# Optimization experiments

Measured on AMD Instinct MI355X. Metric: run time of the kernel, lower is better.

## Reference

```python
import jax, jax.numpy as jnp
import numpy as np

K_NEIGHBORS = 32  # nsample

def setup_inputs() -> dict:
    key = jax.random.key(0)
    ks = jax.random.split(key, 16)
    B, C, N = 4, 3, 4096
    def w(k, shape):
        return jax.random.normal(k, shape, dtype=jnp.float32) * 0.05
    inp = {"x": jax.random.normal(ks[0], (B, C, N), dtype=jnp.float32)}
    # three scale MLPs share shapes -> stack along leading scale axis (s=3)
    inp["sW0"] = w(ks[1], (3, 64, 3));    inp["sb0"] = w(ks[2], (3, 64))
    inp["sW1"] = w(ks[3], (3, 64, 64));   inp["sb1"] = w(ks[4], (3, 64))
    inp["sW2"] = w(ks[5], (3, 128, 64));  inp["sb2"] = w(ks[6], (3, 128))
    inp["gW0"] = w(ks[7], (256, 384));    inp["gb0"] = w(ks[8], (256,))
    inp["gW1"] = w(ks[9], (1024, 256));   inp["gb1"] = w(ks[10], (1024,))
    inp["mW0"] = w(ks[11], (256, 1024));  inp["mb0"] = w(ks[12], (256,))
    inp["mW1"] = w(ks[13], (128, 256));   inp["mb1"] = w(ks[14], (128,))
    return inp

def _knn_idx(x, k):
    # x: [B, 3, N] channels-first points; k nearest neighbors excluding self
    pts = jnp.swapaxes(x, 1, 2)                       # [B, N, 3]
    sq = jnp.sum(pts * pts, axis=-1)                  # [B, N]
    d = sq[:, :, None] + sq[:, None, :] - 2.0 * jnp.einsum('bnc,bmc->bnm', pts, pts)
    _, idx = jax.lax.top_k(-d, k + 1)                 # nearest first (self at 0)
    return idx[:, :, 1:]                              # [B, N, k]

def reference(x, sW0, sb0, sW1, sb1, sW2, sb2, gW0, gb0, gW1, gb1, mW0, mb0, mW1, mb1):
    B, C, N = x.shape
    # radius is unused by sample_and_group_knn -> all three scales share knn idx
    idx = _knn_idx(x, K_NEIGHBORS)                    # [B, N, K]
    # gather: per-batch x[:, idx[b]] -> [B, C, N, K]
    g = jax.vmap(lambda xf, i: xf[:, i])(x, idx)
    # three shared-weight 1x1-conv MLPs, batched over scale axis s
    h = jax.nn.relu(jnp.einsum('bcnk,soc->sbonk', g, sW0) + sb0[:, None, :, None, None])
    h = jax.nn.relu(jnp.einsum('sbcnk,soc->sbonk', h, sW1) + sb1[:, None, :, None, None])
    h = jax.nn.relu(jnp.einsum('sbcnk,soc->sbonk', h, sW2) + sb2[:, None, :, None, None])
    p = jnp.max(h, axis=-1)                           # [3, B, 128, N] max over neighbors
    point = jnp.moveaxis(p, 0, 1).reshape(B, 3 * p.shape[2], N)  # concat scales -> [B, 384, N]
    gf = jax.nn.relu(jnp.einsum('bcn,oc->bon', point, gW0) + gb0[None, :, None])
    gf = jax.nn.relu(jnp.einsum('bcn,oc->bon', gf, gW1) + gb1[None, :, None])     # [B,1024,N]
    msf = jax.nn.relu(jnp.einsum('bcn,oc->bon', gf, mW0) + mb0[None, :, None])
    msf = jax.nn.relu(jnp.einsum('bcn,oc->bon', msf, mW1) + mb1[None, :, None])   # [B,128,N]
    global_feature = jnp.max(gf, axis=-1)             # [B, 1024]
    return (global_feature, msf)
```

## Files before the change

### kernel.cpp

```cpp
#include <hip/hip_runtime.h>
#include <hip/hip_bf16.h>

#define NPTS 4096
#define KNN  32

typedef __attribute__((ext_vector_type(8))) short short8;
typedef __attribute__((ext_vector_type(4))) float floatx4;
typedef unsigned short u16x2 __attribute__((ext_vector_type(2)));

__device__ __forceinline__ unsigned short f2bf(float f) {
    unsigned u = __float_as_uint(f);
    u = (u + 0x7FFFu + ((u >> 16) & 1u)) >> 16;
    return (unsigned short)u;
}

__global__ __launch_bounds__(256) void prep_all(
    const float* __restrict__ x, float4* __restrict__ pts4,
    const float* __restrict__ gW0, const float* __restrict__ gW1,
    const float* __restrict__ mW0, const float* __restrict__ mW1,
    const float* __restrict__ sW1, const float* __restrict__ sW2,
    unsigned short* __restrict__ Wb0, unsigned short* __restrict__ Wb1,
    unsigned short* __restrict__ Wb2, unsigned short* __restrict__ Wb3,
    unsigned short* __restrict__ Wb4, unsigned short* __restrict__ Wb5)
{
    const int blk = blockIdx.x, t = threadIdx.x;
    if (blk < 64) {
        const int i = blk * 256 + t;
        const int b = i >> 12, n = i & (NPTS - 1);
        const float* xb = x + (size_t)b * 3 * NPTS;
        const float qx = xb[n], qy = xb[NPTS + n], qz = xb[2 * NPTS + n];
        pts4[i] = make_float4(qx, qy, qz, qx * qx + qy * qy + qz * qz);
    } else {
        const int wi = (blk - 64) * 256 + t;
        float v; unsigned short* dst;
        if (wi < 98304)       { v = gW0[wi];          dst = Wb0 + wi; }
        else if (wi < 360448) { v = gW1[wi - 98304];  dst = Wb1 + (wi - 98304); }
        else if (wi < 622592) { v = mW0[wi - 360448]; dst = Wb2 + (wi - 360448); }
        else if (wi < 655360) { v = mW1[wi - 622592]; dst = Wb3 + (wi - 622592); }
        else if (wi < 667648) { v = sW1[wi - 655360]; dst = Wb4 + (wi - 655360); }
        else                  { v = sW2[wi - 667648]; dst = Wb5 + (wi - 667648); }
        *dst = f2bf(v);
    }
}

__global__ __launch_bounds__(256) void knn_kernel13(const float4* __restrict__ pts4,
                                                    int* __restrict__ knn_out)
{
    __shared__ unsigned sred[2][4];
    __shared__ unsigned long long C[256];
    __shared__ unsigned ccnt;

    const int t = threadIdx.x, wid = t >> 6, lane = t & 63;
    const int q = blockIdx.x, b = q >> 12, n = q & (NPTS - 1);
    const float4* P = pts4 + ((size_t)b << 12);
    const float4 s = P[n];
    const float px = s.x, py = s.y, pz = s.z, sqn = s.w;

    if (t == 0) ccnt = 0u;

    unsigned key[16];
    #pragma unroll
    for (int g = 0; g < 4; ++g) {
        float4 c0 = P[((g * 4 + 0) << 8) + t];
        float4 c1 = P[((g * 4 + 1) << 8) + t];
        float4 c2 = P[((g * 4 + 2) << 8) + t];
        float4 c3 = P[((g * 4 + 3) << 8) + t];
        float d0 = (sqn + c0.w) - 2.0f * (px * c0.x + py * c0.y + pz * c0.z);
        float d1 = (sqn + c1.w) - 2.0f * (px * c1.x + py * c1.y + pz * c1.z);
        float d2 = (sqn + c2.w) - 2.0f * (px * c2.x + py * c2.y + pz * c2.z);
        float d3 = (sqn + c3.w) - 2.0f * (px * c3.x + py * c3.y + pz * c3.z);
        unsigned u0 = __float_as_uint(d0), u1 = __float_as_uint(d1);
        unsigned u2 = __float_as_uint(d2), u3 = __float_as_uint(d3);
        key[g * 4 + 0] = (u0 & 0x80000000u) ? ~u0 : (u0 | 0x80000000u);
        key[g * 4 + 1] = (u1 & 0x80000000u) ? ~u1 : (u1 | 0x80000000u);
        key[g * 4 + 2] = (u2 & 0x80000000u) ? ~u2 : (u2 | 0x80000000u);
        key[g * 4 + 3] = (u3 & 0x80000000u) ? ~u3 : (u3 | 0x80000000u);
    }

    int pp = 0;
    auto countLE = [&](unsigned thr) -> unsigned {
        unsigned c = 0;
        #pragma unroll
        for (int r = 0; r < 16; ++r)
            c += (unsigned)__popcll(__ballot(key[r] <= thr));
        if (lane == 0) sred[pp & 1][wid] = c;
        __syncthreads();
        const unsigned g = sred[pp & 1][0] + sred[pp & 1][1] +
                           sred[pp & 1][2] + sred[pp & 1][3];
        ++pp;
        return g;
    };

    unsigned lo = 0x100u, hi = 0x1FEu, cntHi = 4096u;
    for (int it = 0; it < 8; ++it) {
        const unsigned mid = (lo + hi) >> 1;
        const unsigned g = countLE((mid << 23) | 0x7FFFFFu);
        if (g >= 33u) { hi = mid; cntHi = g; } else lo = mid + 1u;
    }
    unsigned loK = lo << 23;
    unsigned hiK = (lo << 23) | 0x7FFFFFu;
    unsigned cntF = cntHi;
    while (cntF > 256u && loK < hiK) {
        const unsigned midK = loK + ((hiK - loK) >> 1);
        const unsigned c = countLE(midK);
        if (c >= 33u) { hiK = midK; cntF = c; } else loK = midK + 1u;
    }
    const unsigned thrF = hiK;

    #pragma unroll
    for (int r = 0; r < 16; ++r) {
        if (key[r] <= thrF) {
            unsigned p = atomicAdd(&ccnt, 1u);
            if (p < 256u)
                C[p] = ((unsigned long long)key[r] << 32) |
                       (unsigned)((r << 8) + t);
        }
    }
    __syncthreads();

    int nc = (int)ccnt; if (nc > 256) nc = 256;
    if (t < nc) {
        const unsigned long long me = C[t];
        int rank = 0;
        for (int j = 0; j < nc; ++j) rank += (C[j] < me) ? 1 : 0;
        if (rank >= 1 && rank <= KNN)
            knn_out[(size_t)q * KNN + (rank - 1)] = (int)(me & 0xFFFFFFFFu);
    }
}

__global__ __launch_bounds__(256) void pointmlp_mfma(
    const float* __restrict__ x,
    const float* __restrict__ sW0, const float* __restrict__ sb0,
    const unsigned short* __restrict__ W1b, const float* __restrict__ sb1,
    const unsigned short* __restrict__ W2b, const float* __restrict__ sb2,
    unsigned short* __restrict__ F)
{
    __shared__ __align__(16) unsigned short W1s[64 * 72];
    __shared__ __align__(16) unsigned short W2s[128 * 72];
    __shared__ __align__(16) unsigned short h0T[32 * 72];
    __shared__ __align__(16) unsigned short h1T[32 * 72];
    __shared__ float W0s[192];
    __shared__ float b0s[64], b1s[64], b2s[128];
    __shared__ float pts[3 * 33];

    const int t = threadIdx.x;
    const int s = blockIdx.y;
    const int tile = blockIdx.x;
    const int b = tile >> 7;
    const int j0 = (tile & 127) << 5;
    const float* xb = x + (size_t)b * 3 * NPTS;

    if (t < 192) W0s[t] = sW0[s * 192 + t];
    if (t < 64) b0s[t] = sb0[s * 64 + t];
    if (t >= 64 && t < 128) b1s[t - 64] = sb1[s * 64 + (t - 64)];
    if (t < 128) b2s[t] = sb2[s * 128 + t];
    if (t < 96) { int c = t >> 5, p = t & 31; pts[c * 33 + p] = xb[c * NPTS + j0 + p]; }
    {
        const int o = t & 63, qq = t >> 6;
        const unsigned short* src = W1b + (size_t)s * 4096 + o * 64 + qq * 16;
        *(uint4*)&W1s[o * 72 + qq * 16]     = *(const uint4*)src;
        *(uint4*)&W1s[o * 72 + qq * 16 + 8] = *(const uint4*)(src + 8);
    }
    {
        const int o2 = t & 127, hh = t >> 7;
        const unsigned short* src = W2b + (size_t)s * 8192 + o2 * 64 + hh * 32;
        *(uint4*)&W2s[o2 * 72 + hh * 32]      = *(const uint4*)src;
        *(uint4*)&W2s[o2 * 72 + hh * 32 + 8]  = *(const uint4*)(src + 8);
        *(uint4*)&W2s[o2 * 72 + hh * 32 + 16] = *(const uint4*)(src + 16);
        *(uint4*)&W2s[o2 * 72 + hh * 32 + 24] = *(const uint4*)(src + 24);
    }
    __syncthreads();

    {
        const int p = t & 31, og = t >> 5;
        const float xx = pts[p], yy = pts[33 + p], zz = pts[66 + p];
        unsigned short hv[8];
        #pragma unroll
        for (int r = 0; r < 8; ++r) {
            const int o = og * 8 + r;
            float a = b0s[o] + W0s[o * 3] * xx + W0s[o * 3 + 1] * yy
                    + W0s[o * 3 + 2] * zz;
            hv[r] = f2bf(fmaxf(a, 0.0f));
        }
        *(uint4*)&h0T[p * 72 + og * 8] = *(const uint4*)hv;
    }
    __syncthreads();

    const int w = t >> 6, lane = t & 63, quad = lane >> 4, l15 = lane & 15;

    {
        #pragma unroll
        for (int ni = 0; ni < 2; ++ni) {
            floatx4 acc = (floatx4){0.f, 0.f, 0.f, 0.f};
            #pragma unroll
            for (int k0 = 0; k0 < 2; ++k0) {
                short8 aF = *(const short8*)&W1s[(w * 16 + l15) * 72 + k0 * 32 + quad * 8];
                short8 bF = *(const short8*)&h0T[(ni * 16 + l15) * 72 + k0 * 32 + quad * 8];
                acc = __builtin_amdgcn_mfma_f32_16x16x32_bf16(aF, bF, acc, 0, 0, 0);
            }
            const int m0 = w * 16 + quad * 4;
            const int p = ni * 16 + l15;
            ushort4 pk;
            pk.x = f2bf(fmaxf(acc[0] + b1s[m0 + 0], 0.f));
            pk.y = f2bf(fmaxf(acc[1] + b1s[m0 + 1], 0.f));
            pk.z = f2bf(fmaxf(acc[2] + b1s[m0 + 2], 0.f));
            pk.w = f2bf(fmaxf(acc[3] + b1s[m0 + 3], 0.f));
            *(ushort4*)&h1T[p * 72 + m0] = pk;
        }
    }
    __syncthreads();

    {
        #pragma unroll
        for (int mi = 0; mi < 2; ++mi) {
            const int m0 = (w * 2 + mi) * 16;
            #pragma unroll
            for (int ni = 0; ni < 2; ++ni) {
                floatx4 acc = (floatx4){0.f, 0.f, 0.f, 0.f};
                #pragma unroll
                for (int k0 = 0; k0 < 2; ++k0) {
                    short8 aF = *(const short8*)&W2s[(m0 + l15) * 72 + k0 * 32 + quad * 8];
                    short8 bF = *(const short8*)&h1T[(ni * 16 + l15) * 72 + k0 * 32 + quad * 8];
                    acc = __builtin_amdgcn_mfma_f32_16x16x32_bf16(aF, bF, acc, 0, 0, 0);
                }
                const int o2 = m0 + quad * 4;
                const int j = j0 + ni * 16 + l15;
                ushort4 pk;
                pk.x = f2bf(fmaxf(acc[0] + b2s[o2 + 0], 0.f));
                pk.y = f2bf(fmaxf(acc[1] + b2s[o2 + 1], 0.f));
                pk.z = f2bf(fmaxf(acc[2] + b2s[o2 + 2], 0.f));
                pk.w = f2bf(fmaxf(acc[3] + b2s[o2 + 3], 0.f));
                *(ushort4*)&F[((size_t)b * NPTS + j) * 384 + s * 128 + o2] = pk;
            }
        }
    }
}

__global__ __launch_bounds__(192) void maxgather_bf16(
    const unsigned short* __restrict__ F, const int* __restrict__ knn,
    unsigned short* __restrict__ pt)
{
    __shared__ int idxS[KNN];
    const int q = blockIdx.x;
    const int b = q >> 12;
    const int t = threadIdx.x;
    if (t < KNN) idxS[t] = knn[(size_t)q * KNN + t];
    __syncthreads();
    const unsigned short* Fb = F + (size_t)b * NPTS * 384 + t * 2;
    u16x2 m = (u16x2)0;
    #pragma unroll 8
    for (int k = 0; k < KNN; ++k) {
        u16x2 v = *(const u16x2*)(Fb + (size_t)idxS[k] * 384);
        m = __builtin_elementwise_max(m, v);
    }
    *(u16x2*)(pt + (size_t)q * 384 + t * 2) = m;
}

template<int DO_ROWMAX>
__global__ __launch_bounds__(256) void gemm_bf16(
    const unsigned short* __restrict__ Wb, const unsigned short* __restrict__ Bt,
    const float* __restrict__ bias, void* __restrict__ outp,
    float* __restrict__ gfeat, int M, int K)
{
    __shared__ __align__(16) unsigned short As[128 * 40];
    __shared__ __align__(16) unsigned short Bs[128 * 40];
    __shared__ float biasS[128];
    __shared__ int redI[128];

    const int t = threadIdx.x;
    const int b = blockIdx.z;
    const int m0 = blockIdx.x * 128;
    const int n0 = blockIdx.y * 128;
    if (t < 128) biasS[t] = bias[m0 + t];
    if (DO_ROWMAX && t < 128) redI[t] = 0;

    const int wave = t >> 6, lane = t & 63, quad = lane >> 4, l15 = lane & 15;
    const int wr = wave >> 1, wc = wave & 1;

    const int am = t & 127, akh = t >> 7;
    const unsigned short* Wp = Wb + (size_t)(m0 + am) * K + akh * 16;
    const int bn = t >> 2, bq = t & 3;
    const unsigned short* Bp = Bt + ((size_t)b * NPTS + n0) * K;

    floatx4 acc[16];
    #pragma unroll
    for (int i = 0; i < 16; ++i) acc[i] = (floatx4){0.f, 0.f, 0.f, 0.f};

    const int nk = K >> 5;
    for (int kt = 0; kt < nk; ++kt) {
        const int k0 = kt << 5;
        uint4 av0 = *(const uint4*)(Wp + k0);
        uint4 av1 = *(const uint4*)(Wp + k0 + 8);
        uint4 bv0 = *(const uint4*)(Bp + (size_t)bn * K + k0 + bq * 8);
        uint4 bv1 = *(const uint4*)(Bp + (size_t)(bn + 64) * K + k0 + bq * 8);
        __syncthreads();
        {
            uint4* dst = (uint4*)&As[am * 40 + akh * 16];
            dst[0] = av0;
            dst[1] = av1;
            *(uint4*)&Bs[bn * 40 + bq * 8] = bv0;
            *(uint4*)&Bs[(bn + 64) * 40 + bq * 8] = bv1;
        }
        __syncthreads();
        short8 af[4], bfv[4];
        #pragma unroll
        for (int i = 0; i < 4; ++i)
            af[i] = *(const short8*)&As[(wr * 64 + i * 16 + l15) * 40 + quad * 8];
        #pragma unroll
        for (int j = 0; j < 4; ++j)
            bfv[j] = *(const short8*)&Bs[(wc * 64 + j * 16 + l15) * 40 + quad * 8];
        #pragma unroll
        for (int i = 0; i < 4; ++i)
            #pragma unroll
            for (int j = 0; j < 4; ++j)
                acc[i * 4 + j] = __builtin_amdgcn_mfma_f32_16x16x32_bf16(
                    af[i], bfv[j], acc[i * 4 + j], 0, 0, 0);
    }

    #pragma unroll
    for (int i = 0; i < 4; ++i) {
        const int mbase = wr * 64 + i * 16 + quad * 4;
        float rm0 = 0.f, rm1 = 0.f, rm2 = 0.f, rm3 = 0.f;
        #pragma unroll
        for (int j = 0; j < 4; ++j) {
            const int n = n0 + wc * 64 + j * 16 + l15;
            float v0 = fmaxf(acc[i * 4 + j][0] + biasS[mbase + 0], 0.f);
            float v1 = fmaxf(acc[i * 4 + j][1] + biasS[mbase + 1], 0.f);
            float v2 = fmaxf(acc[i * 4 + j][2] + biasS[mbase + 2], 0.f);
            float v3 = fmaxf(acc[i * 4 + j][3] + biasS[mbase + 3], 0.f);
            if (DO_ROWMAX) {
                rm0 = fmaxf(rm0, v0); rm1 = fmaxf(rm1, v1);
                rm2 = fmaxf(rm2, v2); rm3 = fmaxf(rm3, v3);
            }
            ushort4 pk;
            pk.x = f2bf(v0); pk.y = f2bf(v1); pk.z = f2bf(v2); pk.w = f2bf(v3);
            *(ushort4*)((unsigned short*)outp +
                        ((size_t)b * NPTS + n) * M + m0 + mbase) = pk;
        }
        if (DO_ROWMAX) {
            atomicMax(&redI[mbase + 0], __float_as_int(rm0));
            atomicMax(&redI[mbase + 1], __float_as_int(rm1));
            atomicMax(&redI[mbase + 2], __float_as_int(rm2));
            atomicMax(&redI[mbase + 3], __float_as_int(rm3));
        }
    }
    if (DO_ROWMAX) {
        __syncthreads();
        if (t < 128)
            atomicMax((int*)&gfeat[(size_t)b * 1024 + m0 + t], redI[t]);
    }
}

__global__ __launch_bounds__(256) void fused_head(
    const unsigned short* __restrict__ Wb2, const unsigned short* __restrict__ Wb3,
    const float* __restrict__ mb0, const float* __restrict__ mb1,
    const unsigned short* __restrict__ gft, float* __restrict__ outp)
{
    __shared__ __align__(16) unsigned short As[256 * 40];
    __shared__ __align__(16) unsigned short Bs[64 * 40];
    __shared__ __align__(16) unsigned short H[64 * 264];
    __shared__ float b0s[256];
    __shared__ float b1s[128];

    const int t = threadIdx.x;
    const int n0 = blockIdx.x * 64;
    const int b = blockIdx.y;
    b0s[t] = mb0[t];
    if (t < 128) b1s[t] = mb1[t];

    const int wave = t >> 6, lane = t & 63, quad = lane >> 4, l15 = lane & 15;

    const unsigned short* Ap = Wb2 + (size_t)t * 1024;
    const int bn = t >> 2, bq = t & 3;
    const unsigned short* Bp = gft + ((size_t)b * NPTS + n0) * 1024;

    floatx4 acc[16];
    #pragma unroll
    for (int i = 0; i < 16; ++i) acc[i] = (floatx4){0.f, 0.f, 0.f, 0.f};

    for (int kt = 0; kt < 32; ++kt) {
        const int k0 = kt << 5;
        uint4 a0 = *(const uint4*)(Ap + k0);
        uint4 a1 = *(const uint4*)(Ap + k0 + 8);
        uint4 a2 = *(const uint4*)(Ap + k0 + 16);
        uint4 a3 = *(const uint4*)(Ap + k0 + 24);
        uint4 bv = *(const uint4*)(Bp + (size_t)bn * 1024 + k0 + bq * 8);
        __syncthreads();
        *(uint4*)&As[t * 40 + 0]  = a0;
        *(uint4*)&As[t * 40 + 8]  = a1;
        *(uint4*)&As[t * 40 + 16] = a2;
        *(uint4*)&As[t * 40 + 24] = a3;
        *(uint4*)&Bs[bn * 40 + bq * 8] = bv;
        __syncthreads();
        short8 af[4], bfv[4];
        #pragma unroll
        for (int i = 0; i < 4; ++i)
            af[i] = *(const short8*)&As[(wave * 64 + i * 16 + l15) * 40 + quad * 8];
        #pragma unroll
        for (int j = 0; j < 4; ++j)
            bfv[j] = *(const short8*)&Bs[(j * 16 + l15) * 40 + quad * 8];
        #pragma unroll
        for (int i = 0; i < 4; ++i)
            #pragma unroll
            for (int j = 0; j < 4; ++j)
                acc[i * 4 + j] = __builtin_amdgcn_mfma_f32_16x16x32_bf16(
                    af[i], bfv[j], acc[i * 4 + j], 0, 0, 0);
    }
    #pragma unroll
    for (int i = 0; i < 4; ++i) {
        const int mbase = wave * 64 + i * 16 + quad * 4;
        #pragma unroll
        for (int j = 0; j < 4; ++j) {
            const int nl = j * 16 + l15;
            ushort4 pk;
            pk.x = f2bf(fmaxf(acc[i * 4 + j][0] + b0s[mbase + 0], 0.f));
            pk.y = f2bf(fmaxf(acc[i * 4 + j][1] + b0s[mbase + 1], 0.f));
            pk.z = f2bf(fmaxf(acc[i * 4 + j][2] + b0s[mbase + 2], 0.f));
            pk.w = f2bf(fmaxf(acc[i * 4 + j][3] + b0s[mbase + 3], 0.f));
            *(ushort4*)&H[nl * 264 + mbase] = pk;
        }
    }

    floatx4 acc2[8];
    #pragma unroll
    for (int i = 0; i < 8; ++i) acc2[i] = (floatx4){0.f, 0.f, 0.f, 0.f};
    const int am2 = t & 127, ah = t >> 7;

    for (int kt = 0; kt < 8; ++kt) {
        const int k0 = kt << 5;
        uint4 a0 = *(const uint4*)(Wb3 + (size_t)am2 * 256 + k0 + ah * 16);
        uint4 a1 = *(const uint4*)(Wb3 + (size_t)am2 * 256 + k0 + ah * 16 + 8);
        __syncthreads();
        *(uint4*)&As[am2 * 40 + ah * 16]     = a0;
        *(uint4*)&As[am2 * 40 + ah * 16 + 8] = a1;
        __syncthreads();
        short8 af2[2], bf2[4];
        #pragma unroll
        for (int i = 0; i < 2; ++i)
            af2[i] = *(const short8*)&As[(wave * 32 + i * 16 + l15) * 40 + quad * 8];
        #pragma unroll
        for (int j = 0; j < 4; ++j)
            bf2[j] = *(const short8*)&H[(j * 16 + l15) * 264 + k0 + quad * 8];
        #pragma unroll
        for (int i = 0; i < 2; ++i)
            #pragma unroll
            for (int j = 0; j < 4; ++j)
                acc2[i * 4 + j] = __builtin_amdgcn_mfma_f32_16x16x32_bf16(
                    af2[i], bf2[j], acc2[i * 4 + j], 0, 0, 0);
    }
    #pragma unroll
    for (int i = 0; i < 2; ++i) {
        const int m2 = wave * 32 + i * 16 + quad * 4;
        #pragma unroll
        for (int j = 0; j < 4; ++j) {
            const int n = n0 + j * 16 + l15;
            float* o = outp + ((size_t)b * 128 + m2) * NPTS + n;
            o[0 * NPTS] = fmaxf(acc2[i * 4 + j][0] + b1s[m2 + 0], 0.f);
            o[1 * NPTS] = fmaxf(acc2[i * 4 + j][1] + b1s[m2 + 1], 0.f);
            o[2 * NPTS] = fmaxf(acc2[i * 4 + j][2] + b1s[m2 + 2], 0.f);
            o[3 * NPTS] = fmaxf(acc2[i * 4 + j][3] + b1s[m2 + 3], 0.f);
        }
    }
}

extern "C" void kernel_launch(void* const* d_in, const int* in_sizes, int n_in,
                              void* d_out, int out_size, void* d_ws, size_t ws_size,
                              hipStream_t stream)
{
    const float* x   = (const float*)d_in[0];
    const float* sW0 = (const float*)d_in[1];
    const float* sb0 = (const float*)d_in[2];
    const float* sW1 = (const float*)d_in[3];
    const float* sb1 = (const float*)d_in[4];
    const float* sW2 = (const float*)d_in[5];
    const float* sb2 = (const float*)d_in[6];
    const float* gW0 = (const float*)d_in[7];
    const float* gb0 = (const float*)d_in[8];
    const float* gW1 = (const float*)d_in[9];
    const float* gb1 = (const float*)d_in[10];
    const float* mW0 = (const float*)d_in[11];
    const float* mb0 = (const float*)d_in[12];
    const float* mW1 = (const float*)d_in[13];
    const float* mb1 = (const float*)d_in[14];
    float* outp = (float*)d_out;

    char* ws = (char*)d_ws;
    int*            idx     = (int*)(ws);
    float4*         pts4    = (float4*)(ws + 2097152u);
    unsigned short* Wb0     = (unsigned short*)(ws + 2359296u);
    unsigned short* Wb1     = (unsigned short*)(ws + 2555904u);
    unsigned short* Wb2     = (unsigned short*)(ws + 3080192u);
    unsigned short* Wb3     = (unsigned short*)(ws + 3604480u);
    unsigned short* Wb4     = (unsigned short*)(ws + 3670016u);
    unsigned short* Wb5     = (unsigned short*)(ws + 3694592u);
    unsigned short* F       = (unsigned short*)(ws + 4194304u);
    unsigned short* point_t = (unsigned short*)(ws + 18874368u);
    unsigned short* gf0t    = (unsigned short*)(ws + 33554432u);
    unsigned short* gft     = (unsigned short*)(ws + 50331648u);

    prep_all<<<dim3(2768), dim3(256), 0, stream>>>(
        x, pts4, gW0, gW1, mW0, mW1, sW1, sW2, Wb0, Wb1, Wb2, Wb3, Wb4, Wb5);
    knn_kernel13<<<dim3(16384), dim3(256), 0, stream>>>(pts4, idx);
    pointmlp_mfma<<<dim3(512, 3), dim3(256), 0, stream>>>(
        x, sW0, sb0, Wb4, sb1, Wb5, sb2, F);
    maxgather_bf16<<<dim3(16384), dim3(192), 0, stream>>>(F, idx, point_t);
    gemm_bf16<0><<<dim3(2, 32, 4), dim3(256), 0, stream>>>(
        Wb0, point_t, gb0, gf0t, nullptr, 256, 384);
    gemm_bf16<1><<<dim3(8, 32, 4), dim3(256), 0, stream>>>(
        Wb1, gf0t, gb1, gft, outp, 1024, 256);
    fused_head<<<dim3(64, 4), dim3(256), 0, stream>>>(
        Wb2, Wb3, mb0, mb1, gft, outp + 4096);
}
```

Baseline: 268.5 us.

## Stage batch points in LDS and process multiple kNN queries per block

The kNN kernel now launches 512 blocks of 512 threads. Each block loads its batch's 4096 points into shared memory once, then walks 32 queries, with each 256-thread half handling two queries at a time so the threshold bisection for both shares the ballots and barriers. The old version re-read all points from global memory for every query. In exchange it uses 64KB of LDS per block, has far fewer blocks to spread across CUs, and runs up to 23 extra refinement passes whenever either of the two paired queries needs them.

```diff
diff --git a/kernel.cpp b/kernel.cpp
--- a/kernel.cpp
+++ b/kernel.cpp
@@ -43,88 +43,134 @@
     }
 }
 
-__global__ __launch_bounds__(256) void knn_kernel13(const float4* __restrict__ pts4,
+__global__ __launch_bounds__(512) void knn_kernel14(const float4* __restrict__ pts4,
                                                     int* __restrict__ knn_out)
 {
-    __shared__ unsigned sred[2][4];
-    __shared__ unsigned long long C[256];
-    __shared__ unsigned ccnt;
-
-    const int t = threadIdx.x, wid = t >> 6, lane = t & 63;
-    const int q = blockIdx.x, b = q >> 12, n = q & (NPTS - 1);
+    __shared__ float4 ptsS[NPTS];
+    __shared__ unsigned sredA[2][8], sredB[2][8];
+    __shared__ unsigned long long Cbuf[2][2][256];
+    __shared__ unsigned ccnt[2][2];
+    __shared__ unsigned flags[2];
+
+    const int t    = threadIdx.x;
+    const int h    = t >> 8;
+    const int tl   = t & 255;
+    const int wid  = t >> 6;
+    const int lane = t & 63;
+
+    const int blk = blockIdx.x;
+    const int b   = blk >> 7;
+    const int q0  = (blk & 127) << 5;
+
     const float4* P = pts4 + ((size_t)b << 12);
-    const float4 s = P[n];
-    const float px = s.x, py = s.y, pz = s.z, sqn = s.w;
-
-    if (t == 0) ccnt = 0u;
-
-    unsigned key[16];
-    #pragma unroll
-    for (int g = 0; g < 4; ++g) {
-        float4 c0 = P[((g * 4 + 0) << 8) + t];
-        float4 c1 = P[((g * 4 + 1) << 8) + t];
-        float4 c2 = P[((g * 4 + 2) << 8) + t];
-        float4 c3 = P[((g * 4 + 3) << 8) + t];
-        float d0 = (sqn + c0.w) - 2.0f * (px * c0.x + py * c0.y + pz * c0.z);
-        float d1 = (sqn + c1.w) - 2.0f * (px * c1.x + py * c1.y + pz * c1.z);
-        float d2 = (sqn + c2.w) - 2.0f * (px * c2.x + py * c2.y + pz * c2.z);
-        float d3 = (sqn + c3.w) - 2.0f * (px * c3.x + py * c3.y + pz * c3.z);
-        unsigned u0 = __float_as_uint(d0), u1 = __float_as_uint(d1);
-        unsigned u2 = __float_as_uint(d2), u3 = __float_as_uint(d3);
-        key[g * 4 + 0] = (u0 & 0x80000000u) ? ~u0 : (u0 | 0x80000000u);
-        key[g * 4 + 1] = (u1 & 0x80000000u) ? ~u1 : (u1 | 0x80000000u);
-        key[g * 4 + 2] = (u2 & 0x80000000u) ? ~u2 : (u2 | 0x80000000u);
-        key[g * 4 + 3] = (u3 & 0x80000000u) ? ~u3 : (u3 | 0x80000000u);
-    }
+    #pragma unroll
+    for (int i = 0; i < 8; ++i) ptsS[i * 512 + t] = P[i * 512 + t];
+    __syncthreads();
 
     int pp = 0;
-    auto countLE = [&](unsigned thr) -> unsigned {
-        unsigned c = 0;
-        #pragma unroll
-        for (int r = 0; r < 16; ++r)
-            c += (unsigned)__popcll(__ballot(key[r] <= thr));
-        if (lane == 0) sred[pp & 1][wid] = c;
-        __syncthreads();
-        const unsigned g = sred[pp & 1][0] + sred[pp & 1][1] +
-                           sred[pp & 1][2] + sred[pp & 1][3];
+    auto countLE2 = [&](unsigned ta, unsigned tb, unsigned* kA, unsigned* kB,
+                        unsigned& ga, unsigned& gb) {
+        unsigned ca = 0, cb = 0;
+        #pragma unroll
+        for (int r = 0; r < 16; ++r) {
+            ca += (unsigned)__popcll(__ballot(kA[r] <= ta));
+            cb += (unsigned)__popcll(__ballot(kB[r] <= tb));
+        }
+        if (lane == 0) { sredA[pp & 1][wid] = ca; sredB[pp & 1][wid] = cb; }
+        __syncthreads();
+        const int base = h * 4;
+        ga = sredA[pp & 1][base + 0] + sredA[pp & 1][base + 1] +
+             sredA[pp & 1][base + 2] + sredA[pp & 1][base + 3];
+        gb = sredB[pp & 1][base + 0] + sredB[pp & 1][base + 1] +
+             sredB[pp & 1][base + 2] + sredB[pp & 1][base + 3];
         ++pp;
-        return g;
     };
 
-    unsigned lo = 0x100u, hi = 0x1FEu, cntHi = 4096u;
     for (int it = 0; it < 8; ++it) {
-        const unsigned mid = (lo + hi) >> 1;
-        const unsigned g = countLE((mid << 23) | 0x7FFFFFu);
-        if (g >= 33u) { hi = mid; cntHi = g; } else lo = mid + 1u;
-    }
-    unsigned loK = lo << 23;
-    unsigned hiK = (lo << 23) | 0x7FFFFFu;
-    unsigned cntF = cntHi;
-    while (cntF > 256u && loK < hiK) {
-        const unsigned midK = loK + ((hiK - loK) >> 1);
-        const unsigned c = countLE(midK);
-        if (c >= 33u) { hiK = midK; cntF = c; } else loK = midK + 1u;
-    }
-    const unsigned thrF = hiK;
-
-    #pragma unroll
-    for (int r = 0; r < 16; ++r) {
-        if (key[r] <= thrF) {
-            unsigned p = atomicAdd(&ccnt, 1u);
-            if (p < 256u)
-                C[p] = ((unsigned long long)key[r] << 32) |
-                       (unsigned)((r << 8) + t);
-        }
-    }
-    __syncthreads();
-
-    int nc = (int)ccnt; if (nc > 256) nc = 256;
-    if (t < nc) {
-        const unsigned long long me = C[t];
-        int rank = 0;
-        for (int j = 0; j < nc; ++j) rank += (C[j] < me) ? 1 : 0;
-        if (rank >= 1 && rank <= KNN)
-            knn_out[(size_t)q * KNN + (rank - 1)] = (int)(me & 0xFFFFFFFFu);
+        const int qa = q0 + it * 4 + h * 2;
+        const int qb = qa + 1;
+
+        if (tl == 0) { ccnt[h][0] = 0u; ccnt[h][1] = 0u; }
+
+        const float4 sA = ptsS[qa];
+        const float4 sB = ptsS[qb];
+
+        unsigned kA[16], kB[16];
+        #pragma unroll
+        for (int r = 0; r < 16; ++r) {
+            const float4 c = ptsS[(r << 8) + tl];
+            float dA = (sA.w + c.w) - 2.0f * (sA.x * c.x + sA.y * c.y + sA.z * c.z);
+            float dB = (sB.w + c.w) - 2.0f * (sB.x * c.x + sB.y * c.y + sB.z * c.z);
+            unsigned uA = __float_as_uint(dA), uB = __float_as_uint(dB);
+            kA[r] = (uA & 0x80000000u) ? ~uA : (uA | 0x80000000u);
+            kB[r] = (uB & 0x80000000u) ? ~uB : (uB | 0x80000000u);
+        }
+
+        unsigned loA = 0x100u, hiA = 0x1FEu, cHiA = 4096u;
+        unsigned loB = 0x100u, hiB = 0x1FEu, cHiB = 4096u;
+        for (int i2 = 0; i2 < 8; ++i2) {
+            const unsigned mA = (loA + hiA) >> 1;
+            const unsigned mB = (loB + hiB) >> 1;
+            unsigned ga, gb;
+            countLE2((mA << 23) | 0x7FFFFFu, (mB << 23) | 0x7FFFFFu, kA, kB, ga, gb);
+            if (ga >= 33u) { hiA = mA; cHiA = ga; } else loA = mA + 1u;
+            if (gb >= 33u) { hiB = mB; cHiB = gb; } else loB = mB + 1u;
+        }
+        unsigned loKA = loA << 23, hiKA = (loA << 23) | 0x7FFFFFu, cFA = cHiA;
+        unsigned loKB = loB << 23, hiKB = (loB << 23) | 0x7FFFFFu, cFB = cHiB;
+
+        if (tl == 0) flags[h] = ((cFA > 256u) || (cFB > 256u)) ? 1u : 0u;
+        __syncthreads();
+        if ((flags[0] | flags[1]) != 0u) {
+            for (int i2 = 0; i2 < 23; ++i2) {
+                const bool nA = (cFA > 256u) && (loKA < hiKA);
+                const bool nB = (cFB > 256u) && (loKB < hiKB);
+                const unsigned mA = nA ? (loKA + ((hiKA - loKA) >> 1)) : hiKA;
+                const unsigned mB = nB ? (loKB + ((hiKB - loKB) >> 1)) : hiKB;
+                unsigned ga, gb;
+                countLE2(mA, mB, kA, kB, ga, gb);
+                if (nA) { if (ga >= 33u) { hiKA = mA; cFA = ga; } else loKA = mA + 1u; }
+                if (nB) { if (gb >= 33u) { hiKB = mB; cFB = gb; } else loKB = mB + 1u; }
+            }
+        }
+        const unsigned thrA = hiKA, thrB = hiKB;
+
+        #pragma unroll
+        for (int r = 0; r < 16; ++r) {
+            if (kA[r] <= thrA) {
+                unsigned p = atomicAdd(&ccnt[h][0], 1u);
+                if (p < 256u)
+                    Cbuf[h][0][p] = ((unsigned long long)kA[r] << 32) |
+                                    (unsigned)((r << 8) + tl);
+            }
+            if (kB[r] <= thrB) {
+                unsigned p = atomicAdd(&ccnt[h][1], 1u);
+                if (p < 256u)
+                    Cbuf[h][1][p] = ((unsigned long long)kB[r] << 32) |
+                                    (unsigned)((r << 8) + tl);
+            }
+        }
+        __syncthreads();
+
+        int ncA = (int)ccnt[h][0]; if (ncA > 256) ncA = 256;
+        int ncB = (int)ccnt[h][1]; if (ncB > 256) ncB = 256;
+        if (tl < ncA) {
+            const unsigned long long me = Cbuf[h][0][tl];
+            int rank = 0;
+            for (int j = 0; j < ncA; ++j) rank += (Cbuf[h][0][j] < me) ? 1 : 0;
+            if (rank >= 1 && rank <= KNN)
+                knn_out[((size_t)((b << 12) + qa)) * KNN + (rank - 1)] =
+                    (int)(me & 0xFFFFFFFFu);
+        }
+        if (tl < ncB) {
+            const unsigned long long me = Cbuf[h][1][tl];
+            int rank = 0;
+            for (int j = 0; j < ncB; ++j) rank += (Cbuf[h][1][j] < me) ? 1 : 0;
+            if (rank >= 1 && rank <= KNN)
+                knn_out[((size_t)((b << 12) + qb)) * KNN + (rank - 1)] =
+                    (int)(me & 0xFFFFFFFFu);
+        }
+        __syncthreads();
     }
 }
 
@@ -500,7 +546,7 @@
 
     prep_all<<<dim3(2768), dim3(256), 0, stream>>>(
         x, pts4, gW0, gW1, mW0, mW1, sW1, sW2, Wb0, Wb1, Wb2, Wb3, Wb4, Wb5);
-    knn_kernel13<<<dim3(16384), dim3(256), 0, stream>>>(pts4, idx);
+    knn_kernel14<<<dim3(512), dim3(512), 0, stream>>>(pts4, idx);
     pointmlp_mfma<<<dim3(512, 3), dim3(256), 0, stream>>>(
         x, sW0, sb0, Wb4, sb1, Wb5, sb2, F);
     maxgather_bf16<<<dim3(16384), dim3(192), 0, stream>>>(F, idx, point_t);
```

New measurement: 365.3 us. +36.1%, slower.

## Pick kNN candidate threshold from 33rd-smallest group minimum instead of radix search

Applied to the files above, without the earlier changes.

Each thread first takes the minimum of its 16 distance keys. These are reduced to 64 group minima, and one wave-local ballot binary search finds the 33rd smallest of them. That value is a threshold guaranteed to keep the true 33 nearest points as candidates. It replaces the block-wide bisection over key bits, which needed a __syncthreads per iteration, and keeps the old search only as a fallback when more than 256 candidates pass. The cost is an extra shared array and a 32-step ballot loop, plus rare slow fallbacks on clustered inputs.

```diff
diff --git a/kernel.cpp b/kernel.cpp
--- a/kernel.cpp
+++ b/kernel.cpp
@@ -43,10 +43,11 @@
     }
 }
 
-__global__ __launch_bounds__(256) void knn_kernel13(const float4* __restrict__ pts4,
+__global__ __launch_bounds__(256) void knn_kernel16(const float4* __restrict__ pts4,
                                                     int* __restrict__ knn_out)
 {
     __shared__ unsigned sred[2][4];
+    __shared__ unsigned minS[256];
     __shared__ unsigned long long C[256];
     __shared__ unsigned ccnt;
 
@@ -77,39 +78,31 @@
         key[g * 4 + 3] = (u3 & 0x80000000u) ? ~u3 : (u3 | 0x80000000u);
     }
 
-    int pp = 0;
-    auto countLE = [&](unsigned thr) -> unsigned {
-        unsigned c = 0;
-        #pragma unroll
-        for (int r = 0; r < 16; ++r)
-            c += (unsigned)__popcll(__ballot(key[r] <= thr));
-        if (lane == 0) sred[pp & 1][wid] = c;
-        __syncthreads();
-        const unsigned g = sred[pp & 1][0] + sred[pp & 1][1] +
-                           sred[pp & 1][2] + sred[pp & 1][3];
-        ++pp;
-        return g;
-    };
-
-    unsigned lo = 0x100u, hi = 0x1FEu, cntHi = 4096u;
-    for (int it = 0; it < 8; ++it) {
-        const unsigned mid = (lo + hi) >> 1;
-        const unsigned g = countLE((mid << 23) | 0x7FFFFFu);
-        if (g >= 33u) { hi = mid; cntHi = g; } else lo = mid + 1u;
-    }
-    unsigned loK = lo << 23;
-    unsigned hiK = (lo << 23) | 0x7FFFFFu;
-    unsigned cntF = cntHi;
-    while (cntF > 256u && loK < hiK) {
-        const unsigned midK = loK + ((hiK - loK) >> 1);
-        const unsigned c = countLE(midK);
-        if (c >= 33u) { hiK = midK; cntF = c; } else loK = midK + 1u;
-    }
-    const unsigned thrF = hiK;
+    unsigned tm = key[0];
+    #pragma unroll
+    for (int r = 1; r < 16; ++r) tm = (key[r] < tm) ? key[r] : tm;
+    minS[t] = tm;
+    __syncthreads();
+
+    unsigned m0 = minS[lane];
+    unsigned m1 = minS[lane + 64];
+    unsigned m2 = minS[lane + 128];
+    unsigned m3 = minS[lane + 192];
+    m0 = (m1 < m0) ? m1 : m0;
+    m2 = (m3 < m2) ? m3 : m2;
+    m0 = (m2 < m0) ? m2 : m0;
+
+    unsigned lo = 0u, hi = 0xFFFFFFFFu;
+    for (int i = 0; i < 32; ++i) {
+        const unsigned mid = lo + ((hi - lo) >> 1);
+        const unsigned cnt = (unsigned)__popcll(__ballot(m0 <= mid));
+        if (cnt >= 33u) hi = mid; else lo = mid + 1u;
+    }
+    const unsigned thr0 = hi;
 
     #pragma unroll
     for (int r = 0; r < 16; ++r) {
-        if (key[r] <= thrF) {
+        if (key[r] <= thr0) {
             unsigned p = atomicAdd(&ccnt, 1u);
             if (p < 256u)
                 C[p] = ((unsigned long long)key[r] << 32) |
@@ -118,7 +111,50 @@
     }
     __syncthreads();
 
-    int nc = (int)ccnt; if (nc > 256) nc = 256;
+    int nc = (int)ccnt;
+    if (nc > 256) {
+        if (t == 0) ccnt = 0u;
+        int pp = 0;
+        auto countLE = [&](unsigned thr) -> unsigned {
+            unsigned c = 0;
+            #pragma unroll
+            for (int r = 0; r < 16; ++r)
+                c += (unsigned)__popcll(__ballot(key[r] <= thr));
+            if (lane == 0) sred[pp & 1][wid] = c;
+            __syncthreads();
+            const unsigned g = sred[pp & 1][0] + sred[pp & 1][1] +
+                               sred[pp & 1][2] + sred[pp & 1][3];
+            ++pp;
+            return g;
+        };
+        unsigned lo2 = 0x100u, hi2 = 0x1FEu, cntHi = 4096u;
+        for (int it = 0; it < 8; ++it) {
+            const unsigned mid = (lo2 + hi2) >> 1;
+            const unsigned g = countLE((mid << 23) | 0x7FFFFFu);
+            if (g >= 33u) { hi2 = mid; cntHi = g; } else lo2 = mid + 1u;
+        }
+        unsigned loK = lo2 << 23;
+        unsigned hiK = (lo2 << 23) | 0x7FFFFFu;
+        unsigned cntF = cntHi;
+        while (cntF > 256u && loK < hiK) {
+            const unsigned midK = loK + ((hiK - loK) >> 1);
+            const unsigned c = countLE(midK);
+            if (c >= 33u) { hiK = midK; cntF = c; } else loK = midK + 1u;
+        }
+        const unsigned thrF = hiK;
+        #pragma unroll
+        for (int r = 0; r < 16; ++r) {
+            if (key[r] <= thrF) {
+                unsigned p = atomicAdd(&ccnt, 1u);
+                if (p < 256u)
+                    C[p] = ((unsigned long long)key[r] << 32) |
+                           (unsigned)((r << 8) + t);
+            }
+        }
+        __syncthreads();
+        nc = (int)ccnt; if (nc > 256) nc = 256;
+    }
+
     if (t < nc) {
         const unsigned long long me = C[t];
         int rank = 0;
@@ -500,7 +536,7 @@
 
     prep_all<<<dim3(2768), dim3(256), 0, stream>>>(
         x, pts4, gW0, gW1, mW0, mW1, sW1, sW2, Wb0, Wb1, Wb2, Wb3, Wb4, Wb5);
-    knn_kernel13<<<dim3(16384), dim3(256), 0, stream>>>(pts4, idx);
+    knn_kernel16<<<dim3(16384), dim3(256), 0, stream>>>(pts4, idx);
     pointmlp_mfma<<<dim3(512, 3), dim3(256), 0, stream>>>(
         x, sW0, sb0, Wb4, sb1, Wb5, sb2, F);
     maxgather_bf16<<<dim3(16384), dim3(192), 0, stream>>>(F, idx, point_t);
```

After: 250.8 us. 1.07x faster.
